# Kernel optimization log

Measured on AMD Instinct MI355X. Metric: run time of the kernel, lower is better.

## Reference

```python
import jax, jax.numpy as jnp
import numpy as np

NEG_SLOPE = 0.2  # PyG GATConv default negative_slope
N_NODES = 4096
N_EDGES = 32768
IN_CH = 128
HID = 512
OUT_CH = 10
HEADS = 8


def gat_conv(x, src, dst, W, a_src, a_dst, bias, num_nodes):
    """PyG-style GATConv (eval mode, self-loops already in src/dst).
    x: [N, F_in], W: [F_in, H*C], a_src/a_dst: [H, C], bias: [H*C].
    Returns concat-heads output [N, H*C]."""
    H, C = a_src.shape
    h = (x @ W).reshape(num_nodes, H, C)                      # [N,H,C]
    alpha_src = jnp.sum(h * a_src, axis=-1)                   # [N,H]
    alpha_dst = jnp.sum(h * a_dst, axis=-1)                   # [N,H]
    e = alpha_src[src] + alpha_dst[dst]                       # [E,H] per-edge logits
    e = jnp.where(e > 0, e, NEG_SLOPE * e)                    # leaky_relu
    # segment softmax over incoming edges of each dst node (self-loops => non-empty)
    m = jax.ops.segment_max(e, dst, num_segments=num_nodes)   # [N,H]
    e = jnp.exp(e - m[dst])
    denom = jax.ops.segment_sum(e, dst, num_segments=num_nodes)
    alpha = e / denom[dst]                                    # [E,H]
    msg = h[src] * alpha[:, :, None]                          # [E,H,C] gather+weight
    out = jax.ops.segment_sum(msg, dst, num_segments=num_nodes)  # scatter-add
    return out.reshape(num_nodes, H * C) + bias


def setup_inputs() -> dict:
    key = jax.random.key(0)
    ks = jax.random.split(key, 16)
    s = 0.05
    inp = {
        "x": jax.random.normal(ks[0], (N_NODES, IN_CH), jnp.float32),
        "edge_index": jax.random.randint(ks[1], (2, N_EDGES), 0, N_NODES, jnp.int64),
        "edge_attr": jax.random.normal(ks[2], (N_EDGES, 16), jnp.float32),
        "W1": jax.random.normal(ks[3], (IN_CH, HEADS * HID), jnp.float32) * s,
        "a_src1": jax.random.normal(ks[4], (HEADS, HID), jnp.float32) * s,
        "a_dst1": jax.random.normal(ks[5], (HEADS, HID), jnp.float32) * s,
        "b1": jnp.zeros((HEADS * HID,), jnp.float32),
        "W2": jax.random.normal(ks[6], (HEADS * HID, HID), jnp.float32) * s,
        "a_src2": jax.random.normal(ks[7], (1, HID), jnp.float32) * s,
        "a_dst2": jax.random.normal(ks[8], (1, HID), jnp.float32) * s,
        "b2": jnp.zeros((HID,), jnp.float32),
        # MLP head
        "fc1_w": jax.random.normal(ks[9], (4096, 512), jnp.float32) * s,
        "fc1_b": jnp.zeros((512,), jnp.float32),
        "fc2_w": jax.random.normal(ks[10], (512, 128), jnp.float32) * s,
        "fc2_b": jnp.zeros((128,), jnp.float32),
        "fc3_w": jax.random.normal(ks[11], (128, OUT_CH), jnp.float32) * s,
        "fc3_b": jnp.zeros((OUT_CH,), jnp.float32),
    }
    return inp


def reference(x, edge_index, edge_attr, W1, a_src1, a_dst1, b1, W2, a_src2, a_dst2, b2,
              fc1_w, fc1_b, fc2_w, fc2_b, fc3_w, fc3_b):
    # edge_attr is ignored: GATConv was built without edge_dim (lin_edge is None in PyG).
    del edge_attr
    n = x.shape[0]
    loops = jnp.arange(n, dtype=edge_index.dtype)
    src = jnp.concatenate([edge_index[0], loops])  # add_self_loops=True default
    dst = jnp.concatenate([edge_index[1], loops])
    h = jax.nn.relu(gat_conv(x, src, dst, W1, a_src1, a_dst1, b1, n))   # [N, 4096]
    h = jax.nn.relu(gat_conv(h, src, dst, W2, a_src2, a_dst2, b2, n))   # [N, 512]
    g = h.reshape(-1, 8 * h.shape[-1])                                   # [N/8, 4096]
    g = jax.nn.relu(g @ fc1_w + fc1_b)
    g = jax.nn.relu(g @ fc2_w + fc2_b)
    return g @ fc3_w + fc3_b                                             # [N/8, 10]
```

## Files before the change

kernel.cpp:

```cpp
#include <hip/hip_runtime.h>
#include <cstdint>
#include <cstddef>

#define NN    4096
#define E0C   32768
#define ETC   (E0C+NN)
#define HC1   8
#define CC    512
#define F_IN  128
#define NEG_SLOPE_F 0.2f
#define ELLW  64

typedef __bf16 bf16_t;
typedef __bf16 bf16x8 __attribute__((ext_vector_type(8)));
typedef __bf16 bf16x4 __attribute__((ext_vector_type(4)));
typedef __bf16 bf16x2 __attribute__((ext_vector_type(2)));
typedef float  f32x4  __attribute__((ext_vector_type(4)));

__device__ __forceinline__ void tcast_body(const float* __restrict__ W, bf16_t* __restrict__ Wt,
                                           int K, int N, int bx, int by)
{
    __shared__ float t[32][33];
    int bn = bx * 32, bk = by * 32;
    int tx = threadIdx.x & 31, ty = threadIdx.x >> 5;
    #pragma unroll
    for (int i = 0; i < 32; i += 8)
        t[ty + i][tx] = W[(size_t)(bk + ty + i) * N + bn + tx];
    __syncthreads();
    #pragma unroll
    for (int i = 0; i < 32; i += 8)
        Wt[(size_t)(bn + ty + i) * K + bk + tx] = (bf16_t)t[tx][ty + i];
}

__global__ __launch_bounds__(256) void prep_k(const float* __restrict__ x,
    const float* __restrict__ W1, const float* __restrict__ W2,
    const float* __restrict__ fc1w, const float* __restrict__ a_src1,
    const float* __restrict__ a_dst1, const int* __restrict__ ei,
    bf16_t* __restrict__ x_bf, bf16_t* __restrict__ Wt1, bf16_t* __restrict__ Wt2,
    bf16_t* __restrict__ fc1wt, bf16_t* __restrict__ w1sT,
    int* __restrict__ srcELL, int* __restrict__ indeg)
{
    const int b = blockIdx.x;
    if (b < 512) {
        int i = (b * 256 + threadIdx.x) * 4;
        float4 v = *(const float4*)&x[i];
        bf16x4 o;
        o[0] = (bf16_t)v.x; o[1] = (bf16_t)v.y; o[2] = (bf16_t)v.z; o[3] = (bf16_t)v.w;
        *(bf16x4*)&x_bf[i] = o;
    } else if (b < 1024) {
        int bl = b - 512;
        tcast_body(W1, Wt1, F_IN, 4096, bl % 128, bl / 128);
    } else if (b < 3072) {
        int bl = b - 1024;
        tcast_body(W2, Wt2, 4096, 512, bl % 16, bl / 16);
    } else if (b < 5120) {
        int bl = b - 3072;
        tcast_body(fc1w, fc1wt, 4096, 512, bl % 16, bl / 16);
    } else if (b < 5152) {
        int bl = b - 5120;
        int wave = threadIdx.x >> 6, lane = threadIdx.x & 63;
        int k = bl * 4 + wave;
        int hd = lane >> 3;
        int co = (lane & 7) * 64;
        const float* wrow = W1 + (size_t)k * (HC1 * CC) + hd * CC + co;
        const float* vs = a_src1 + hd * CC + co;
        const float* vd = a_dst1 + hd * CC + co;
        float s = 0.f, d = 0.f;
        #pragma unroll 4
        for (int t = 0; t < 64; ++t) {
            float w = wrow[t];
            s += w * vs[t];
            d += w * vd[t];
        }
        #pragma unroll
        for (int off = 1; off < 8; off <<= 1) {
            s += __shfl_xor(s, off);
            d += __shfl_xor(d, off);
        }
        if ((lane & 7) == 0) {
            w1sT[hd * F_IN + k]       = (bf16_t)s;
            w1sT[(hd + 8) * F_IN + k] = (bf16_t)d;
        }
    } else {
        int e = (b - 5152) * 256 + threadIdx.x;
        if (e < ETC) {
            int s, d;
            if (e < E0C) { s = ei[e]; d = ei[E0C + e]; }
            else         { s = e - E0C; d = s; }
            int pos = atomicAdd(&indeg[d], 1);
            if (pos < ELLW) srcELL[d * ELLW + pos] = s;
        }
    }
}

__global__ __launch_bounds__(256) void alpha1_k(const bf16_t* __restrict__ x_bf,
                                                const bf16_t* __restrict__ w1sT,
                                                float* __restrict__ as1, float* __restrict__ ad1)
{
    const int wave = threadIdx.x >> 6, lane = threadIdx.x & 63;
    const int bm = blockIdx.x * 64 + wave * 16;
    const int lm = lane & 15, quad = lane >> 4;
    f32x4 acc = {};
    #pragma unroll
    for (int k0 = 0; k0 < F_IN; k0 += 32) {
        bf16x8 af = *(const bf16x8*)&x_bf[(size_t)(bm + lm) * F_IN + k0 + quad * 8];
        bf16x8 bf = *(const bf16x8*)&w1sT[lm * F_IN + k0 + quad * 8];
        acc = __builtin_amdgcn_mfma_f32_16x16x32_bf16(af, bf, acc, 0, 0, 0);
    }
    #pragma unroll
    for (int r = 0; r < 4; ++r) {
        int n = bm + quad * 4 + r;
        if (lm < 8) as1[n * HC1 + lm] = acc[r];
        else        ad1[n * HC1 + (lm - 8)] = acc[r];
    }
}

__global__ __launch_bounds__(256) void aggx_k(const bf16_t* __restrict__ x_bf,
    const float* __restrict__ as1, const float* __restrict__ ad1,
    const int* __restrict__ indeg, const int* __restrict__ srcELL,
    bf16_t* __restrict__ xagg)
{
    const int wave = threadIdx.x >> 6, lane = threadIdx.x & 63;
    const int n = blockIdx.x * 4 + wave;
    const int c = lane * 2;
    const int deg = min(indeg[n], ELLW);

    int vsrc = 0;
    float vp[HC1] = {};
    if (lane < deg) {
        vsrc = srcELL[n * ELLW + lane];
        #pragma unroll
        for (int hd = 0; hd < HC1; ++hd) {
            float v = as1[vsrc * HC1 + hd] + ad1[n * HC1 + hd];
            v = (v > 0.f) ? v : NEG_SLOPE_F * v;
            vp[hd] = __expf(v);
        }
    }
    #pragma unroll
    for (int hd = 0; hd < HC1; ++hd) {
        float dsum = vp[hd];
        #pragma unroll
        for (int off = 1; off < 64; off <<= 1)
            dsum += __shfl_xor(dsum, off);
        vp[hd] *= 1.f / dsum;
    }

    float acc[HC1][2] = {};
    for (int ii = 0; ii < deg; ++ii) {
        int s = __shfl(vsrc, ii);
        bf16x2 rv = *(const bf16x2*)&x_bf[(size_t)s * F_IN + c];
        float r0 = (float)rv[0], r1 = (float)rv[1];
        #pragma unroll
        for (int hd = 0; hd < HC1; ++hd) {
            float al = __shfl(vp[hd], ii);
            acc[hd][0] += al * r0;
            acc[hd][1] += al * r1;
        }
    }
    #pragma unroll
    for (int hd = 0; hd < HC1; ++hd) {
        bf16x2 o;
        o[0] = (bf16_t)acc[hd][0];
        o[1] = (bf16_t)acc[hd][1];
        *(bf16x2*)&xagg[((size_t)n * HC1 + hd) * F_IN + c] = o;
    }
}

__global__ __launch_bounds__(256, 2) void gemmh_k(const bf16_t* __restrict__ xagg,
                                                  const bf16_t* __restrict__ Wt1,
                                                  const float* __restrict__ b1,
                                                  bf16_t* __restrict__ out1)
{
    __shared__ bf16_t As[128 * 32];
    __shared__ bf16_t Bs[128 * 32];
    const int tid = threadIdx.x;
    const int bm = blockIdx.x * 128, bn = blockIdx.y * 128;
    const int hd = blockIdx.z;

    const int wave = tid >> 6, lane = tid & 63;
    const int wm = wave >> 1, wn = wave & 1;
    const int lm = lane & 15, quad = lane >> 4;

    const int sr = tid >> 2;
    const int kg = tid & 3;
    const int swz = ((kg ^ (sr & 3)) * 8);

    const bf16_t* Aptr = xagg + ((size_t)(bm + sr) * HC1 + hd) * F_IN + kg * 8;
    const bf16_t* Bptr = Wt1 + (size_t)(hd * CC + bn + sr) * F_IN + kg * 8;
    const size_t raskip = (size_t)64 * HC1 * F_IN;
    const size_t rbskip = (size_t)64 * F_IN;

    bf16x8 ra0 = *(const bf16x8*)(Aptr);
    bf16x8 ra1 = *(const bf16x8*)(Aptr + raskip);
    bf16x8 rb0 = *(const bf16x8*)(Bptr);
    bf16x8 rb1 = *(const bf16x8*)(Bptr + rbskip);

    f32x4 acc[4][4] = {};

    for (int k0 = 0; k0 < F_IN; k0 += 32) {
        __syncthreads();
        *(bf16x8*)&As[sr * 32 + swz]        = ra0;
        *(bf16x8*)&As[(sr + 64) * 32 + swz] = ra1;
        *(bf16x8*)&Bs[sr * 32 + swz]        = rb0;
        *(bf16x8*)&Bs[(sr + 64) * 32 + swz] = rb1;
        __syncthreads();
        if (k0 + 32 < F_IN) {
            Aptr += 32; Bptr += 32;
            ra0 = *(const bf16x8*)(Aptr);
            ra1 = *(const bf16x8*)(Aptr + raskip);
            rb0 = *(const bf16x8*)(Bptr);
            rb1 = *(const bf16x8*)(Bptr + rbskip);
        }
        const int fswz = ((quad ^ (lm & 3)) * 8);
        bf16x8 af[4], bfr[4];
        #pragma unroll
        for (int i = 0; i < 4; ++i) {
            af[i]  = *(const bf16x8*)&As[(wm * 64 + i * 16 + lm) * 32 + fswz];
            bfr[i] = *(const bf16x8*)&Bs[(wn * 64 + i * 16 + lm) * 32 + fswz];
        }
        #pragma unroll
        for (int mt = 0; mt < 4; ++mt)
            #pragma unroll
            for (int nt = 0; nt < 4; ++nt)
                acc[mt][nt] = __builtin_amdgcn_mfma_f32_16x16x32_bf16(af[mt], bfr[nt], acc[mt][nt], 0, 0, 0);
    }

    #pragma unroll
    for (int nt = 0; nt < 4; ++nt) {
        int gc = bn + wn * 64 + nt * 16 + lm;
        float bv = b1[hd * CC + gc];
        #pragma unroll
        for (int mt = 0; mt < 4; ++mt)
            #pragma unroll
            for (int r = 0; r < 4; ++r) {
                int gr = bm + wm * 64 + mt * 16 + quad * 4 + r;
                out1[(size_t)gr * 4096 + hd * CC + gc] = (bf16_t)fmaxf(acc[mt][nt][r] + bv, 0.f);
            }
    }
}

__global__ __launch_bounds__(256, 2) void gemm128s_k(const bf16_t* __restrict__ A,
                                                     const bf16_t* __restrict__ Bt,
                                                     bf16_t* __restrict__ Cpart,
                                                     int M, int N, int K, int Kc)
{
    __shared__ bf16_t As[128 * 32];
    __shared__ bf16_t Bs[128 * 32];
    const int tid = threadIdx.x;
    const int bm = blockIdx.x * 128, bn = blockIdx.y * 128;
    const int kz = blockIdx.z;
    const int k_beg = kz * Kc;
    const int k_end = k_beg + Kc;

    const int wave = tid >> 6, lane = tid & 63;
    const int wm = wave >> 1, wn = wave & 1;
    const int lm = lane & 15, quad = lane >> 4;

    const int sr = tid >> 2;
    const int kg = tid & 3;
    const int swz = ((kg ^ (sr & 3)) * 8);

    const bf16_t* Aptr = A + (size_t)(bm + sr) * K + k_beg + kg * 8;
    const bf16_t* Bptr = Bt + (size_t)(bn + sr) * K + k_beg + kg * 8;
    const size_t rowskip = (size_t)64 * K;

    bf16x8 ra0 = *(const bf16x8*)(Aptr);
    bf16x8 ra1 = *(const bf16x8*)(Aptr + rowskip);
    bf16x8 rb0 = *(const bf16x8*)(Bptr);
    bf16x8 rb1 = *(const bf16x8*)(Bptr + rowskip);

    f32x4 acc[4][4] = {};

    for (int k0 = k_beg; k0 < k_end; k0 += 32) {
        __syncthreads();
        *(bf16x8*)&As[sr * 32 + swz]        = ra0;
        *(bf16x8*)&As[(sr + 64) * 32 + swz] = ra1;
        *(bf16x8*)&Bs[sr * 32 + swz]        = rb0;
        *(bf16x8*)&Bs[(sr + 64) * 32 + swz] = rb1;
        __syncthreads();
        if (k0 + 32 < k_end) {
            Aptr += 32; Bptr += 32;
            ra0 = *(const bf16x8*)(Aptr);
            ra1 = *(const bf16x8*)(Aptr + rowskip);
            rb0 = *(const bf16x8*)(Bptr);
            rb1 = *(const bf16x8*)(Bptr + rowskip);
        }
        const int fswz = ((quad ^ (lm & 3)) * 8);
        bf16x8 af[4], bfr[4];
        #pragma unroll
        for (int i = 0; i < 4; ++i) {
            af[i]  = *(const bf16x8*)&As[(wm * 64 + i * 16 + lm) * 32 + fswz];
            bfr[i] = *(const bf16x8*)&Bs[(wn * 64 + i * 16 + lm) * 32 + fswz];
        }
        #pragma unroll
        for (int mt = 0; mt < 4; ++mt)
            #pragma unroll
            for (int nt = 0; nt < 4; ++nt)
                acc[mt][nt] = __builtin_amdgcn_mfma_f32_16x16x32_bf16(af[mt], bfr[nt], acc[mt][nt], 0, 0, 0);
    }

    bf16_t* P = Cpart + (size_t)kz * M * N;
    #pragma unroll
    for (int nt = 0; nt < 4; ++nt) {
        int gc = bn + wn * 64 + nt * 16 + lm;
        #pragma unroll
        for (int mt = 0; mt < 4; ++mt)
            #pragma unroll
            for (int r = 0; r < 4; ++r) {
                int gr = bm + wm * 64 + mt * 16 + quad * 4 + r;
                P[(size_t)gr * N + gc] = (bf16_t)acc[mt][nt][r];
            }
    }
}

__global__ __launch_bounds__(256) void reduce_h2_k(const bf16_t* __restrict__ P,
    const float* __restrict__ a_s, const float* __restrict__ a_d,
    bf16_t* __restrict__ h2bf, float* __restrict__ as2, float* __restrict__ ad2)
{
    __shared__ float sred[4][2];
    const int t = threadIdx.x;
    const int i = blockIdx.x * 1024 + t * 4;
    f32x4 s = {};
    #pragma unroll
    for (int z = 0; z < 4; ++z) {
        bf16x4 pv = *(const bf16x4*)&P[(size_t)z * NN * CC + i];
        #pragma unroll
        for (int j = 0; j < 4; ++j) s[j] += (float)pv[j];
    }
    bf16x4 o;
    #pragma unroll
    for (int j = 0; j < 4; ++j) o[j] = (bf16_t)s[j];
    *(bf16x4*)&h2bf[i] = o;

    const int c = (t & 127) * 4;
    f32x4 va = *(const f32x4*)&a_s[c];
    f32x4 vd = *(const f32x4*)&a_d[c];
    float ls = s[0]*va[0] + s[1]*va[1] + s[2]*va[2] + s[3]*va[3];
    float ld = s[0]*vd[0] + s[1]*vd[1] + s[2]*vd[2] + s[3]*vd[3];
    #pragma unroll
    for (int off = 32; off > 0; off >>= 1) {
        ls += __shfl_down(ls, off);
        ld += __shfl_down(ld, off);
    }
    const int wave = t >> 6, lane = t & 63;
    if (lane == 0) { sred[wave][0] = ls; sred[wave][1] = ld; }
    __syncthreads();
    if (t == 0) {
        as2[blockIdx.x * 2]     = sred[0][0] + sred[1][0];
        ad2[blockIdx.x * 2]     = sred[0][1] + sred[1][1];
    }
    if (t == 128) {
        as2[blockIdx.x * 2 + 1] = sred[2][0] + sred[3][0];
        ad2[blockIdx.x * 2 + 1] = sred[2][1] + sred[3][1];
    }
}

__global__ __launch_bounds__(128) void tail_k(const bf16_t* __restrict__ P,
                                              const float* __restrict__ fc1b,
                                              const float* __restrict__ fc2w,
                                              const float* __restrict__ fc2b,
                                              const float* __restrict__ fc3w,
                                              const float* __restrict__ fc3b,
                                              float* __restrict__ out)
{
    __shared__ float sA[512];
    __shared__ float sF2[128];
    const int m = blockIdx.x, t = threadIdx.x;
    const int MN = 512 * 512;
    #pragma unroll
    for (int i = 0; i < 4; ++i) {
        int c = t + i * 128;
        float v = 0.f;
        #pragma unroll
        for (int z = 0; z < 16; ++z)
            v += (float)P[(size_t)z * MN + (size_t)m * 512 + c];
        sA[c] = fmaxf(v + fc1b[c], 0.f);
    }
    __syncthreads();
    float a0 = 0.f, a1 = 0.f, a2 = 0.f, a3 = 0.f;
    #pragma unroll 4
    for (int k = 0; k < 512; k += 4) {
        a0 += sA[k + 0] * fc2w[(k + 0) * 128 + t];
        a1 += sA[k + 1] * fc2w[(k + 1) * 128 + t];
        a2 += sA[k + 2] * fc2w[(k + 2) * 128 + t];
        a3 += sA[k + 3] * fc2w[(k + 3) * 128 + t];
    }
    sF2[t] = fmaxf((a0 + a1) + (a2 + a3) + fc2b[t], 0.f);
    __syncthreads();
    if (t < 10) {
        float o = fc3b[t];
        #pragma unroll 4
        for (int k = 0; k < 128; ++k)
            o += sF2[k] * fc3w[k * 10 + t];
        out[(size_t)m * 10 + t] = o;
    }
}

__global__ __launch_bounds__(256) void aggregate2_k(const bf16_t* __restrict__ hbuf,
    const float* __restrict__ as, const float* __restrict__ ad,
    const int* __restrict__ indeg, const int* __restrict__ srcELL,
    const float* __restrict__ bias, bf16_t* __restrict__ outb)
{
    const int g = blockIdx.x;
    const int wave = threadIdx.x >> 6, lane = threadIdx.x & 63;
    const int n = g * 4 + wave;
    const int c = lane * 8;

    const int deg = min(indeg[n], ELLW);
    const float adn = ad[n];

    int vsrc = 0; float vp = 0.f;
    if (lane < deg) {
        vsrc = srcELL[n * ELLW + lane];
        float v = as[vsrc] + adn;
        v = (v > 0.f) ? v : NEG_SLOPE_F * v;
        vp = __expf(v);
    }
    float denom = vp;
    #pragma unroll
    for (int off = 1; off < 64; off <<= 1)
        denom += __shfl_xor(denom, off);
    vp *= 1.f / denom;

    float acc[8] = {};
    int ii = 0;
    for (; ii + 4 <= deg; ii += 4) {
        int s0 = __shfl(vsrc, ii),     s1 = __shfl(vsrc, ii + 1);
        int s2 = __shfl(vsrc, ii + 2), s3 = __shfl(vsrc, ii + 3);
        float a0 = __shfl(vp, ii),     a1 = __shfl(vp, ii + 1);
        float a2 = __shfl(vp, ii + 2), a3 = __shfl(vp, ii + 3);
        bf16x8 r0 = *(const bf16x8*)&hbuf[(size_t)s0 * CC + c];
        bf16x8 r1 = *(const bf16x8*)&hbuf[(size_t)s1 * CC + c];
        bf16x8 r2 = *(const bf16x8*)&hbuf[(size_t)s2 * CC + c];
        bf16x8 r3 = *(const bf16x8*)&hbuf[(size_t)s3 * CC + c];
        #pragma unroll
        for (int j = 0; j < 8; ++j) {
            acc[j] += a0 * (float)r0[j];
            acc[j] += a1 * (float)r1[j];
            acc[j] += a2 * (float)r2[j];
            acc[j] += a3 * (float)r3[j];
        }
    }
    for (; ii < deg; ++ii) {
        int s = __shfl(vsrc, ii);
        float al = __shfl(vp, ii);
        bf16x8 rv = *(const bf16x8*)&hbuf[(size_t)s * CC + c];
        #pragma unroll
        for (int j = 0; j < 8; ++j)
            acc[j] += al * (float)rv[j];
    }
    size_t ob = (size_t)n * CC;
    bf16x8 o;
    #pragma unroll
    for (int j = 0; j < 8; ++j)
        o[j] = (bf16_t)fmaxf(acc[j] + bias[c + j], 0.f);
    *(bf16x8*)&outb[ob + c] = o;
}

extern "C" void kernel_launch(void* const* d_in, const int* in_sizes, int n_in,
                              void* d_out, int out_size, void* d_ws, size_t ws_size,
                              hipStream_t stream) {
    const float* x      = (const float*)d_in[0];
    const int*   ei     = (const int*)d_in[1];
    const float* W1     = (const float*)d_in[3];
    const float* a_src1 = (const float*)d_in[4];
    const float* a_dst1 = (const float*)d_in[5];
    const float* b1     = (const float*)d_in[6];
    const float* W2     = (const float*)d_in[7];
    const float* a_src2 = (const float*)d_in[8];
    const float* a_dst2 = (const float*)d_in[9];
    const float* b2     = (const float*)d_in[10];
    const float* fc1w   = (const float*)d_in[11];
    const float* fc1b   = (const float*)d_in[12];
    const float* fc2w   = (const float*)d_in[13];
    const float* fc2b   = (const float*)d_in[14];
    const float* fc3w   = (const float*)d_in[15];
    const float* fc3b   = (const float*)d_in[16];
    float* out = (float*)d_out;

    char* ws = (char*)d_ws;
    size_t o = 0;
    auto take = [&](size_t bytes) -> char* {
        char* p = ws + o;
        o = (o + bytes + 255) & ~(size_t)255;
        return p;
    };
    int*    indeg  = (int*)take(NN * 4);
    size_t zero_bytes = o;
    float*  as2    = (float*)take(NN * 4);
    float*  ad2    = (float*)take(NN * 4);
    int*    srcELL = (int*)take((size_t)NN * ELLW * 4);
    float*  as1    = (float*)take((size_t)NN * HC1 * 4);
    float*  ad1    = (float*)take((size_t)NN * HC1 * 4);
    bf16_t* w1sT   = (bf16_t*)take((size_t)16 * F_IN * 2);
    bf16_t* x_bf   = (bf16_t*)take((size_t)NN * F_IN * 2);
    bf16_t* xagg   = (bf16_t*)take((size_t)NN * HC1 * F_IN * 2);
    bf16_t* Wt1    = (bf16_t*)take((size_t)F_IN * 4096 * 2);
    bf16_t* Wt2    = (bf16_t*)take((size_t)4096 * 512 * 2);
    bf16_t* fc1wt  = (bf16_t*)take((size_t)4096 * 512 * 2);
    bf16_t* out1bf = (bf16_t*)take((size_t)NN * 4096 * 2);
    bf16_t* h2bf   = (bf16_t*)take((size_t)NN * 512 * 2);
    bf16_t* out2bf = (bf16_t*)take((size_t)NN * 512 * 2);
    bf16_t* part   = (bf16_t*)take((size_t)4 * NN * 512 * 2);

    hipMemsetAsync(d_ws, 0, zero_bytes, stream);

    prep_k<<<dim3(5296), dim3(256), 0, stream>>>(x, W1, W2, fc1w, a_src1, a_dst1, ei,
                                                 x_bf, Wt1, Wt2, fc1wt, w1sT,
                                                 srcELL, indeg);

    alpha1_k<<<dim3(64), dim3(256), 0, stream>>>(x_bf, w1sT, as1, ad1);
    aggx_k<<<dim3(NN / 4), dim3(256), 0, stream>>>(x_bf, as1, ad1, indeg, srcELL, xagg);
    gemmh_k<<<dim3(32, 4, 8), dim3(256), 0, stream>>>(xagg, Wt1, b1, out1bf);

    gemm128s_k<<<dim3(32, 4, 4), dim3(256), 0, stream>>>(
        out1bf, Wt2, part, 4096, 512, 4096, 1024);
    reduce_h2_k<<<dim3(NN / 2), dim3(256), 0, stream>>>(
        part, a_src2, a_dst2, h2bf, as2, ad2);
    aggregate2_k<<<dim3(NN / 4), dim3(256), 0, stream>>>(
        h2bf, as2, ad2, indeg, srcELL, b2, out2bf);

    gemm128s_k<<<dim3(4, 4, 16), dim3(256), 0, stream>>>(
        out2bf, fc1wt, part, 512, 512, 4096, 256);
    tail_k<<<dim3(512), dim3(128), 0, stream>>>(
        part, fc1b, fc2w, fc2b, fc3w, fc3b, out);
}
```

Measured before the change: 206.9 us.

## Fuse split-K reduction and attention logits into GEMM2 via last-block ticket

The separate reduce_h2_k launch is removed. The split-K GEMM for layer 2 now uses a per-tile atomic ticket, so the last of the four K-slice blocks sums the partials, writes h2, and atomically accumulates the src/dst attention logits. This is meant to save a kernel launch and a full pass over the partials, at the cost of atomics, a serial tail in the last block, and a nondeterministic float summation order. The aggx inner loop is also unrolled by two to overlap the gather loads.

```diff
diff --git a/kernel.cpp b/kernel.cpp
--- a/kernel.cpp
+++ b/kernel.cpp
@@ -146,7 +146,22 @@
     }
 
     float acc[HC1][2] = {};
-    for (int ii = 0; ii < deg; ++ii) {
+    int ii = 0;
+    for (; ii + 2 <= deg; ii += 2) {
+        int s0 = __shfl(vsrc, ii), s1 = __shfl(vsrc, ii + 1);
+        bf16x2 r0 = *(const bf16x2*)&x_bf[(size_t)s0 * F_IN + c];
+        bf16x2 r1 = *(const bf16x2*)&x_bf[(size_t)s1 * F_IN + c];
+        float f00 = (float)r0[0], f01 = (float)r0[1];
+        float f10 = (float)r1[0], f11 = (float)r1[1];
+        #pragma unroll
+        for (int hd = 0; hd < HC1; ++hd) {
+            float a0 = __shfl(vp[hd], ii);
+            float a1 = __shfl(vp[hd], ii + 1);
+            acc[hd][0] += a0 * f00 + a1 * f10;
+            acc[hd][1] += a0 * f01 + a1 * f11;
+        }
+    }
+    for (; ii < deg; ++ii) {
         int s = __shfl(vsrc, ii);
         bf16x2 rv = *(const bf16x2*)&x_bf[(size_t)s * F_IN + c];
         float r0 = (float)rv[0], r1 = (float)rv[1];
@@ -239,11 +254,17 @@
     }
 }
 
-__global__ __launch_bounds__(256, 2) void gemm128s_k(const bf16_t* __restrict__ A,
-                                                     const bf16_t* __restrict__ Bt,
-                                                     bf16_t* __restrict__ Cpart,
-                                                     int M, int N, int K, int Kc)
-{
+__global__ __launch_bounds__(256, 2) void gemm2f_k(const bf16_t* __restrict__ A,
+                                                   const bf16_t* __restrict__ Bt,
+                                                   bf16_t* __restrict__ Cpart,
+                                                   int* __restrict__ ticket,
+                                                   const float* __restrict__ a_s,
+                                                   const float* __restrict__ a_d,
+                                                   bf16_t* __restrict__ h2out,
+                                                   float* __restrict__ as2,
+                                                   float* __restrict__ ad2)
+{
+    const int M = NN, N = CC, K = 4096, Kc = 1024;
     __shared__ bf16_t As[128 * 32];
     __shared__ bf16_t Bs[128 * 32];
     const int tid = threadIdx.x;
@@ -311,47 +332,116 @@
                 P[(size_t)gr * N + gc] = (bf16_t)acc[mt][nt][r];
             }
     }
-}
-
-__global__ __launch_bounds__(256) void reduce_h2_k(const bf16_t* __restrict__ P,
-    const float* __restrict__ a_s, const float* __restrict__ a_d,
-    bf16_t* __restrict__ h2bf, float* __restrict__ as2, float* __restrict__ ad2)
-{
-    __shared__ float sred[4][2];
-    const int t = threadIdx.x;
-    const int i = blockIdx.x * 1024 + t * 4;
-    f32x4 s = {};
-    #pragma unroll
-    for (int z = 0; z < 4; ++z) {
-        bf16x4 pv = *(const bf16x4*)&P[(size_t)z * NN * CC + i];
-        #pragma unroll
-        for (int j = 0; j < 4; ++j) s[j] += (float)pv[j];
-    }
-    bf16x4 o;
-    #pragma unroll
-    for (int j = 0; j < 4; ++j) o[j] = (bf16_t)s[j];
-    *(bf16x4*)&h2bf[i] = o;
-
-    const int c = (t & 127) * 4;
-    f32x4 va = *(const f32x4*)&a_s[c];
-    f32x4 vd = *(const f32x4*)&a_d[c];
-    float ls = s[0]*va[0] + s[1]*va[1] + s[2]*va[2] + s[3]*va[3];
-    float ld = s[0]*vd[0] + s[1]*vd[1] + s[2]*vd[2] + s[3]*vd[3];
-    #pragma unroll
-    for (int off = 32; off > 0; off >>= 1) {
-        ls += __shfl_down(ls, off);
-        ld += __shfl_down(ld, off);
-    }
-    const int wave = t >> 6, lane = t & 63;
-    if (lane == 0) { sred[wave][0] = ls; sred[wave][1] = ld; }
+
+    __threadfence();
     __syncthreads();
-    if (t == 0) {
-        as2[blockIdx.x * 2]     = sred[0][0] + sred[1][0];
-        ad2[blockIdx.x * 2]     = sred[0][1] + sred[1][1];
-    }
-    if (t == 128) {
-        as2[blockIdx.x * 2 + 1] = sred[2][0] + sred[3][0];
-        ad2[blockIdx.x * 2 + 1] = sred[2][1] + sred[3][1];
+    __shared__ int s_old;
+    if (tid == 0) s_old = atomicAdd(&ticket[blockIdx.x * 4 + blockIdx.y], 1);
+    __syncthreads();
+    if (s_old != 3) return;
+    __threadfence();
+
+    #pragma unroll
+    for (int mt = 0; mt < 4; ++mt) {
+        #pragma unroll
+        for (int r = 0; r < 4; ++r) {
+            const int gr = bm + wm * 64 + mt * 16 + quad * 4 + r;
+            float rs = 0.f, rd = 0.f;
+            #pragma unroll
+            for (int nt = 0; nt < 4; ++nt) {
+                int gc = bn + wn * 64 + nt * 16 + lm;
+                float v = 0.f;
+                #pragma unroll
+                for (int z = 0; z < 4; ++z)
+                    v += (float)Cpart[(size_t)z * M * N + (size_t)gr * N + gc];
+                h2out[(size_t)gr * N + gc] = (bf16_t)v;
+                rs += v * a_s[gc];
+                rd += v * a_d[gc];
+            }
+            #pragma unroll
+            for (int off = 1; off < 16; off <<= 1) {
+                rs += __shfl_xor(rs, off);
+                rd += __shfl_xor(rd, off);
+            }
+            if (lm == 0) {
+                atomicAdd(&as2[gr], rs);
+                atomicAdd(&ad2[gr], rd);
+            }
+        }
+    }
+}
+
+__global__ __launch_bounds__(256, 2) void gemm128s_k(const bf16_t* __restrict__ A,
+                                                     const bf16_t* __restrict__ Bt,
+                                                     bf16_t* __restrict__ Cpart,
+                                                     int M, int N, int K, int Kc)
+{
+    __shared__ bf16_t As[128 * 32];
+    __shared__ bf16_t Bs[128 * 32];
+    const int tid = threadIdx.x;
+    const int bm = blockIdx.x * 128, bn = blockIdx.y * 128;
+    const int kz = blockIdx.z;
+    const int k_beg = kz * Kc;
+    const int k_end = k_beg + Kc;
+
+    const int wave = tid >> 6, lane = tid & 63;
+    const int wm = wave >> 1, wn = wave & 1;
+    const int lm = lane & 15, quad = lane >> 4;
+
+    const int sr = tid >> 2;
+    const int kg = tid & 3;
+    const int swz = ((kg ^ (sr & 3)) * 8);
+
+    const bf16_t* Aptr = A + (size_t)(bm + sr) * K + k_beg + kg * 8;
+    const bf16_t* Bptr = Bt + (size_t)(bn + sr) * K + k_beg + kg * 8;
+    const size_t rowskip = (size_t)64 * K;
+
+    bf16x8 ra0 = *(const bf16x8*)(Aptr);
+    bf16x8 ra1 = *(const bf16x8*)(Aptr + rowskip);
+    bf16x8 rb0 = *(const bf16x8*)(Bptr);
+    bf16x8 rb1 = *(const bf16x8*)(Bptr + rowskip);
+
+    f32x4 acc[4][4] = {};
+
+    for (int k0 = k_beg; k0 < k_end; k0 += 32) {
+        __syncthreads();
+        *(bf16x8*)&As[sr * 32 + swz]        = ra0;
+        *(bf16x8*)&As[(sr + 64) * 32 + swz] = ra1;
+        *(bf16x8*)&Bs[sr * 32 + swz]        = rb0;
+        *(bf16x8*)&Bs[(sr + 64) * 32 + swz] = rb1;
+        __syncthreads();
+        if (k0 + 32 < k_end) {
+            Aptr += 32; Bptr += 32;
+            ra0 = *(const bf16x8*)(Aptr);
+            ra1 = *(const bf16x8*)(Aptr + rowskip);
+            rb0 = *(const bf16x8*)(Bptr);
+            rb1 = *(const bf16x8*)(Bptr + rowskip);
+        }
+        const int fswz = ((quad ^ (lm & 3)) * 8);
+        bf16x8 af[4], bfr[4];
+        #pragma unroll
+        for (int i = 0; i < 4; ++i) {
+            af[i]  = *(const bf16x8*)&As[(wm * 64 + i * 16 + lm) * 32 + fswz];
+            bfr[i] = *(const bf16x8*)&Bs[(wn * 64 + i * 16 + lm) * 32 + fswz];
+        }
+        #pragma unroll
+        for (int mt = 0; mt < 4; ++mt)
+            #pragma unroll
+            for (int nt = 0; nt < 4; ++nt)
+                acc[mt][nt] = __builtin_amdgcn_mfma_f32_16x16x32_bf16(af[mt], bfr[nt], acc[mt][nt], 0, 0, 0);
+    }
+
+    bf16_t* P = Cpart + (size_t)kz * M * N;
+    #pragma unroll
+    for (int nt = 0; nt < 4; ++nt) {
+        int gc = bn + wn * 64 + nt * 16 + lm;
+        #pragma unroll
+        for (int mt = 0; mt < 4; ++mt)
+            #pragma unroll
+            for (int r = 0; r < 4; ++r) {
+                int gr = bm + wm * 64 + mt * 16 + quad * 4 + r;
+                P[(size_t)gr * N + gc] = (bf16_t)acc[mt][nt][r];
+            }
     }
 }
 
@@ -486,9 +576,10 @@
         return p;
     };
     int*    indeg  = (int*)take(NN * 4);
-    size_t zero_bytes = o;
     float*  as2    = (float*)take(NN * 4);
     float*  ad2    = (float*)take(NN * 4);
+    int*    ticket = (int*)take(128 * 4);
+    size_t zero_bytes = o;
     int*    srcELL = (int*)take((size_t)NN * ELLW * 4);
     float*  as1    = (float*)take((size_t)NN * HC1 * 4);
     float*  ad1    = (float*)take((size_t)NN * HC1 * 4);
@@ -513,10 +604,8 @@
     aggx_k<<<dim3(NN / 4), dim3(256), 0, stream>>>(x_bf, as1, ad1, indeg, srcELL, xagg);
     gemmh_k<<<dim3(32, 4, 8), dim3(256), 0, stream>>>(xagg, Wt1, b1, out1bf);
 
-    gemm128s_k<<<dim3(32, 4, 4), dim3(256), 0, stream>>>(
-        out1bf, Wt2, part, 4096, 512, 4096, 1024);
-    reduce_h2_k<<<dim3(NN / 2), dim3(256), 0, stream>>>(
-        part, a_src2, a_dst2, h2bf, as2, ad2);
+    gemm2f_k<<<dim3(32, 4, 4), dim3(256), 0, stream>>>(
+        out1bf, Wt2, part, ticket, a_src2, a_dst2, h2bf, as2, ad2);
     aggregate2_k<<<dim3(NN / 4), dim3(256), 0, stream>>>(
         h2bf, as2, ad2, indeg, srcELL, b2, out2bf);
 
```

New measurement: 289.2 us. 1.4x slower.
